# Kernel optimization log

Hardware: AMD Instinct MI355X
Metric: run time of the kernel (lower is better)

Reference implementation:

```python
import jax, jax.numpy as jnp
import numpy as np

EMBED_DIM = 512
NUM_HEADS = 8
HEAD_DIM = EMBED_DIM // NUM_HEADS
SCALE = 1.0 / HEAD_DIM ** 0.5


def setup_inputs() -> dict:
    key = jax.random.key(0)
    ks = jax.random.split(key, 7)
    B, C, H, W = 8, EMBED_DIM, 32, 32
    x = jax.random.normal(ks[0], (B, C, H, W), dtype=jnp.float32)
    s = 1.0 / np.sqrt(EMBED_DIM)
    return {
        "x": x,
        "ln_gamma": jnp.ones((EMBED_DIM,), jnp.float32),
        "ln_beta": jnp.zeros((EMBED_DIM,), jnp.float32),
        "w_qkv": jax.random.uniform(ks[1], (EMBED_DIM, 3 * EMBED_DIM), jnp.float32, -s, s),
        "b_qkv": jax.random.uniform(ks[2], (3 * EMBED_DIM,), jnp.float32, -s, s),
        "w_proj": jax.random.uniform(ks[3], (EMBED_DIM, EMBED_DIM), jnp.float32, -s, s),
        "b_proj": jax.random.uniform(ks[4], (EMBED_DIM,), jnp.float32, -s, s),
    }


def reference(x, ln_gamma, ln_beta, w_qkv, b_qkv, w_proj, b_proj):
    B, C, H, W = x.shape
    N = H * W
    # LayerNorm over channel dim (applied in NHWC layout in the original)
    xs = x.reshape(B, C, N).transpose(0, 2, 1)  # [B, N, C]
    mu = jnp.mean(xs, axis=-1, keepdims=True)
    var = jnp.mean(jnp.square(xs - mu), axis=-1, keepdims=True)
    xn = (xs - mu) / jnp.sqrt(var + 1e-5) * ln_gamma + ln_beta
    # QKV projection
    qkv = xn @ w_qkv + b_qkv                        # [B, N, 3C]
    qkv = qkv.reshape(B, N, 3, NUM_HEADS, HEAD_DIM)
    q = qkv[:, :, 0].transpose(0, 2, 1, 3)         # [B, h, N, d]
    k = qkv[:, :, 1].transpose(0, 2, 1, 3)
    v = qkv[:, :, 2].transpose(0, 2, 1, 3)
    # Scaled dot-product attention (full N x N scores, as in source)
    attn = jnp.einsum('bhnd,bhmd->bhnm', q, k) * SCALE
    attn = jax.nn.softmax(attn, axis=-1)
    o = jnp.einsum('bhnm,bhmd->bhnd', attn, v)     # [B, h, N, d]
    o = o.transpose(0, 2, 1, 3).reshape(B, N, C)
    # Output projection (dropout is identity in eval)
    o = o @ w_proj + b_proj
    return o.transpose(0, 2, 1).reshape(B, C, H, W)
```

## Files before the change

kernel.cpp:

```cpp
#include <hip/hip_runtime.h>
#include <hip/hip_bf16.h>
#include <math.h>

#define B_   8
#define C_   512
#define NH_  8
#define HD_  64
#define NSP  1024
#define M_   (B_*NSP)
#define NQKV 1536
#define SCALE_ 0.125f
#define S2L_  0.18033688f

typedef __attribute__((ext_vector_type(8))) __bf16 bf16x8;
typedef __attribute__((ext_vector_type(4))) float  f32x4;
typedef __attribute__((ext_vector_type(16))) float f32x16;

__device__ __forceinline__ unsigned short f2bf(float f) {
  unsigned int u = __float_as_uint(f);
  u = u + 0x7fffu + ((u >> 16) & 1u);
  return (unsigned short)(u >> 16);
}

__device__ __forceinline__ unsigned int pk2bf(float a, float b) {
  __hip_bfloat162 t = __float22bfloat162_rn(make_float2(a, b));
  unsigned int u; __builtin_memcpy(&u, &t, 4);
  return u;
}

__device__ __forceinline__ void async16(const unsigned short* g, unsigned short* l) {
  __builtin_amdgcn_global_load_lds(
      (const __attribute__((address_space(1))) void*)g,
      (__attribute__((address_space(3))) void*)l, 16, 0, 0);
}

__global__ void ln_stats_kernel(const float* __restrict__ x,
                                float* __restrict__ psum,
                                float* __restrict__ psum2) {
  int tx = threadIdx.x & 31, ty = threadIdx.x >> 5;
  int cg  = blockIdx.x & 3;
  int nch = (blockIdx.x >> 2) & 31;
  int b   = blockIdx.x >> 7;
  int n0 = nch * 32;
  const float* xp = x + (size_t)b * C_ * NSP + n0 + tx;
  float s = 0.f, s2 = 0.f;
  for (int c = cg * 128 + ty; c < cg * 128 + 128; c += 8) {
    float v = xp[(size_t)c * NSP];
    s += v; s2 += v * v;
  }
  __shared__ float sh_s[8][32], sh_s2[8][32];
  sh_s[ty][tx] = s; sh_s2[ty][tx] = s2;
  __syncthreads();
  if (ty == 0) {
    float S = 0.f, S2 = 0.f;
    for (int j = 0; j < 8; j++) { S += sh_s[j][tx]; S2 += sh_s2[j][tx]; }
    psum [cg * M_ + b * NSP + n0 + tx] = S;
    psum2[cg * M_ + b * NSP + n0 + tx] = S2;
  }
}

__global__ __launch_bounds__(256) void applyw_kernel(
    const float* __restrict__ x, const float* __restrict__ psum,
    const float* __restrict__ psum2, const float* __restrict__ gamma,
    const float* __restrict__ beta, const float* __restrict__ wqkv,
    const float* __restrict__ wproj, unsigned short* __restrict__ xn,
    unsigned short* __restrict__ wqkvT, unsigned short* __restrict__ wprojT) {
  int tid = threadIdx.x;
  __shared__ float tile[64][65];
  int tx = tid & 63, ty = tid >> 6;
  if (blockIdx.x >= 1024) {
    const float* W; unsigned short* WT; int NW, t;
    if (blockIdx.x < 1216) { W = wqkv;  WT = wqkvT;  NW = NQKV; t = blockIdx.x - 1024; }
    else                   { W = wproj; WT = wprojT; NW = C_;   t = blockIdx.x - 1216; }
    int ntiles = NW >> 6;
    int kt = t / ntiles, nt = t - kt * ntiles;
    for (int i = ty; i < 64; i += 4)
      tile[i][tx] = W[(size_t)(kt * 64 + i) * NW + nt * 64 + tx];
    __syncthreads();
    for (int i = ty; i < 64; i += 4)
      WT[(size_t)(nt * 64 + i) * C_ + kt * 64 + tx] = f2bf(tile[tx][i]);
    return;
  }
  __shared__ float smu[64], srs[64];
  int c0 = (blockIdx.x & 7) * 64;
  int n0 = ((blockIdx.x >> 3) & 15) * 64;
  int b  = blockIdx.x >> 7;
  if (tid < 64) {
    int n = b * NSP + n0 + tid;
    float s  = psum [n] + psum [M_ + n] + psum [2 * M_ + n] + psum [3 * M_ + n];
    float s2 = psum2[n] + psum2[M_ + n] + psum2[2 * M_ + n] + psum2[3 * M_ + n];
    float mu = s * (1.0f / C_);
    float var = s2 * (1.0f / C_) - mu * mu;
    smu[tid] = mu;
    srs[tid] = rsqrtf(var + 1e-5f);
  }
  const float* xp = x + ((size_t)b * C_ + c0) * NSP + n0;
  for (int i = ty; i < 64; i += 4)
    tile[i][tx] = xp[(size_t)i * NSP + tx];
  __syncthreads();
  float g = gamma[c0 + tx], be = beta[c0 + tx];
  unsigned short* op = xn + ((size_t)(b * NSP + n0)) * C_ + c0 + tx;
  for (int i = ty; i < 64; i += 4) {
    float v = (tile[tx][i] - smu[i]) * srs[i] * g + be;
    op[(size_t)i * C_] = f2bf(v);
  }
}

__global__ __launch_bounds__(256) void gemm_qkv_kernel(
    const unsigned short* __restrict__ A,
    const unsigned short* __restrict__ Bt,
    const float* __restrict__ bias,
    unsigned short* __restrict__ out0, unsigned short* __restrict__ out1) {
  __shared__ __align__(16) char smem[24576];
  int tid = threadIdx.x;
  int wave = tid >> 6, lane = tid & 63, quad = lane >> 4, l15 = lane & 15;
  int n0 = blockIdx.x * 128, m0 = blockIdx.y * 64;
  int wm = (wave >> 1) * 32, wn = (wave & 1) * 64;
  int srow = lane >> 2, schunk = (lane & 3) * 8;
  auto stage = [&](int k0, int buf) {
    unsigned short* As = (unsigned short*)(smem + buf * 12288);
    unsigned short* Bs = (unsigned short*)(smem + buf * 12288 + 4096);
    async16(A + (size_t)(m0 + wave * 16 + srow) * 512 + k0 + schunk,
            As + wave * 16 * 32 + lane * 8);
#pragma unroll
    for (int j = 0; j < 2; j++) {
      int r0 = (wave + 4 * j) * 16;
      async16(Bt + (size_t)(n0 + r0 + srow) * 512 + k0 + schunk, Bs + r0 * 32 + lane * 8);
    }
  };
  f32x4 acc[2][4] = {};
  stage(0, 0);
  for (int kt = 0; kt < 16; kt++) {
    int cur = kt & 1;
    __syncthreads();
    if (kt < 15) stage((kt + 1) * 32, cur ^ 1);
    unsigned short* As = (unsigned short*)(smem + cur * 12288);
    unsigned short* Bs = (unsigned short*)(smem + cur * 12288 + 4096);
    bf16x8 a[2], bb[4];
#pragma unroll
    for (int mt = 0; mt < 2; mt++)
      a[mt] = *(const bf16x8*)(As + (wm + mt * 16 + l15) * 32 + quad * 8);
#pragma unroll
    for (int nt = 0; nt < 4; nt++)
      bb[nt] = *(const bf16x8*)(Bs + (wn + nt * 16 + l15) * 32 + quad * 8);
#pragma unroll
    for (int mt = 0; mt < 2; mt++)
#pragma unroll
      for (int nt = 0; nt < 4; nt++)
        acc[mt][nt] = __builtin_amdgcn_mfma_f32_16x16x32_bf16(
            a[mt], bb[nt], acc[mt][nt], 0, 0, 0);
  }
  if (n0 < 1024) {
    float sc = ((n0 + wn) < 512) ? S2L_ : 1.0f;
#pragma unroll
    for (int mt = 0; mt < 2; mt++)
#pragma unroll
      for (int nt = 0; nt < 4; nt++)
#pragma unroll
        for (int r = 0; r < 4; r++) {
          int row = m0 + wm + mt * 16 + quad * 4 + r;
          int col = n0 + wn + nt * 16 + l15;
          out0[(size_t)row * 1024 + col] = f2bf((acc[mt][nt][r] + bias[col]) * sc);
        }
  } else {
    __syncthreads();
    unsigned short* buf = (unsigned short*)smem + wave * (32 * 17);
    int b = m0 >> 10, nbase = m0 & 1023;
    for (int nc = 0; nc < 4; nc++) {
#pragma unroll
      for (int mt = 0; mt < 2; mt++)
#pragma unroll
        for (int r = 0; r < 4; r++) {
          int col = n0 + wn + nc * 16 + l15;
          buf[(mt * 16 + quad * 4 + r) * 17 + l15] = f2bf(acc[mt][nc][r] + bias[col]);
        }
      int ml = lane & 31;
#pragma unroll
      for (int j = 0; j < 8; j++) {
        int cl = j * 2 + (lane >> 5);
        int crel = n0 - 1024 + wn + nc * 16 + cl;
        out1[((size_t)b * C_ + crel) * NSP + nbase + wm + ml] = buf[ml * 17 + cl];
      }
    }
  }
}

__global__ __launch_bounds__(256) void gemm_proj_kernel(
    const unsigned short* __restrict__ A,
    const unsigned short* __restrict__ Bt,
    const float* __restrict__ bias,
    float* __restrict__ O) {
  __shared__ __align__(16) char smem[20480];
  int tid = threadIdx.x;
  int wave = tid >> 6, lane = tid & 63, quad = lane >> 4, l15 = lane & 15;
  int n0 = blockIdx.x * 128, m0 = blockIdx.y * 32;
  int wm = (wave >> 1) * 16, wn = (wave & 1) * 64;
  int srow = lane >> 2, schunk = (lane & 3) * 8;
  auto stage = [&](int k0, int buf) {
    unsigned short* As = (unsigned short*)(smem + buf * 10240);
    unsigned short* Bs = (unsigned short*)(smem + buf * 10240 + 2048);
    if (wave < 2)
      async16(A + (size_t)(m0 + wave * 16 + srow) * 512 + k0 + schunk,
              As + wave * 16 * 32 + lane * 8);
#pragma unroll
    for (int j = 0; j < 2; j++) {
      int r0 = (wave + 4 * j) * 16;
      async16(Bt + (size_t)(n0 + r0 + srow) * 512 + k0 + schunk, Bs + r0 * 32 + lane * 8);
    }
  };
  f32x4 acc[4] = {};
  stage(0, 0);
  for (int kt = 0; kt < 16; kt++) {
    int cur = kt & 1;
    __syncthreads();
    if (kt < 15) stage((kt + 1) * 32, cur ^ 1);
    unsigned short* As = (unsigned short*)(smem + cur * 10240);
    unsigned short* Bs = (unsigned short*)(smem + cur * 10240 + 2048);
    bf16x8 a, bb[4];
    a = *(const bf16x8*)(As + (wm + l15) * 32 + quad * 8);
#pragma unroll
    for (int nt = 0; nt < 4; nt++)
      bb[nt] = *(const bf16x8*)(Bs + (wn + nt * 16 + l15) * 32 + quad * 8);
#pragma unroll
    for (int nt = 0; nt < 4; nt++)
      acc[nt] = __builtin_amdgcn_mfma_f32_16x16x32_bf16(a, bb[nt], acc[nt], 0, 0, 0);
  }
  __syncthreads();
  float* buf = (float*)smem + wave * (16 * 17);
  int b = m0 >> 10, nbase = m0 & 1023;
  int ml = lane & 15, cg = lane >> 4;
  for (int nc = 0; nc < 4; nc++) {
#pragma unroll
    for (int r = 0; r < 4; r++) {
      int col = n0 + wn + nc * 16 + l15;
      buf[(quad * 4 + r) * 17 + l15] = acc[nc][r] + bias[col];
    }
#pragma unroll
    for (int j = 0; j < 4; j++) {
      int cl = j * 4 + cg;
      int c = n0 + wn + nc * 16 + cl;
      O[((size_t)b * C_ + c) * NSP + nbase + wm + ml] = buf[ml * 17 + cl];
    }
  }
}

__global__ __launch_bounds__(256, 2) void attn_kernel(
    const unsigned short* __restrict__ qk,
    const unsigned short* __restrict__ vt,
    unsigned short* __restrict__ o_ws) {
  __shared__ __align__(16) unsigned short Ks[2][64][64];
  __shared__ __align__(16) unsigned short Vts[2][64][64];
  int tid = threadIdx.x;
  int wave = tid >> 6, lane = tid & 63;
  int l31 = lane & 31, hi = lane >> 5;
  int b = blockIdx.x >> 3, h = blockIdx.x & 7;
  int qb = blockIdx.y * 128 + wave * 32;
  int sc8 = lane & 7, sr8 = lane >> 3;
  int swz = sc8 ^ sr8;
  bf16x8 bq[4];
#pragma unroll
  for (int ks = 0; ks < 4; ks++)
    bq[ks] = *(const bf16x8*)(
        qk + (size_t)(b * NSP + qb + l31) * 1024 + h * 64 + ks * 16 + hi * 8);
  auto stage = [&](int it, int buf) {
    int k0 = it * 64;
#pragma unroll
    for (int g = 0; g < 2; g++) {
      int row = wave * 16 + g * 8 + sr8;
      async16(qk + (size_t)(b * NSP + k0 + row) * 1024 + 512 + h * 64 + swz * 8,
              &Ks[buf][wave * 16 + g * 8][0]);
      async16(vt + ((size_t)(b * C_ + h * 64 + row)) * NSP + k0 + swz * 8,
              &Vts[buf][wave * 16 + g * 8][0]);
    }
  };
  f32x16 ot0 = {}, ot1 = {};
  float lsum = 0.f;
  stage(0, 0);
  for (int it = 0; it < 16; it++) {
    int cur = it & 1;
    __syncthreads();
    if (it < 15) stage(it + 1, cur ^ 1);
    bf16x8 bp[4];
#pragma unroll
    for (int kt = 0; kt < 2; kt++) {
      f32x16 s = {};
#pragma unroll
      for (int ks = 0; ks < 4; ks++) {
        bf16x8 ak = *(const bf16x8*)(
            &Ks[cur][kt * 32 + l31][((ks * 2 + hi) ^ (l31 & 7)) * 8]);
        s = __builtin_amdgcn_mfma_f32_32x32x16_bf16(ak, bq[ks], s, 0, 0, 0);
      }
      float p0 = __builtin_amdgcn_exp2f(s[0]),  p1 = __builtin_amdgcn_exp2f(s[1]);
      float p2 = __builtin_amdgcn_exp2f(s[2]),  p3 = __builtin_amdgcn_exp2f(s[3]);
      float p4 = __builtin_amdgcn_exp2f(s[4]),  p5 = __builtin_amdgcn_exp2f(s[5]);
      float p6 = __builtin_amdgcn_exp2f(s[6]),  p7 = __builtin_amdgcn_exp2f(s[7]);
      float p8 = __builtin_amdgcn_exp2f(s[8]),  p9 = __builtin_amdgcn_exp2f(s[9]);
      float pa = __builtin_amdgcn_exp2f(s[10]), pb = __builtin_amdgcn_exp2f(s[11]);
      float pc = __builtin_amdgcn_exp2f(s[12]), pd = __builtin_amdgcn_exp2f(s[13]);
      float pe = __builtin_amdgcn_exp2f(s[14]), pf = __builtin_amdgcn_exp2f(s[15]);
      lsum += ((p0 + p1) + (p2 + p3)) + ((p4 + p5) + (p6 + p7)) +
              (((p8 + p9) + (pa + pb)) + ((pc + pd) + (pe + pf)));
      unsigned int d0 = pk2bf(p0, p1), d1 = pk2bf(p2, p3);
      unsigned int d2 = pk2bf(p4, p5), d3 = pk2bf(p6, p7);
      unsigned int d4 = pk2bf(p8, p9), d5 = pk2bf(pa, pb);
      unsigned int d6 = pk2bf(pc, pd), d7 = pk2bf(pe, pf);
      asm volatile("v_permlane32_swap_b32 %0, %1" : "+v"(d0), "+v"(d2));
      asm volatile("v_permlane32_swap_b32 %0, %1" : "+v"(d1), "+v"(d3));
      asm volatile("v_permlane32_swap_b32 %0, %1" : "+v"(d4), "+v"(d6));
      asm volatile("v_permlane32_swap_b32 %0, %1" : "+v"(d5), "+v"(d7));
      uint4 f0 = make_uint4(d0, d1, d2, d3);
      uint4 f1 = make_uint4(d4, d5, d6, d7);
      __builtin_memcpy(&bp[kt * 2 + 0], &f0, 16);
      __builtin_memcpy(&bp[kt * 2 + 1], &f1, 16);
    }
#pragma unroll
    for (int kc = 0; kc < 4; kc++) {
      bf16x8 av0 = *(const bf16x8*)(
          &Vts[cur][l31][((kc * 2 + hi) ^ (l31 & 7)) * 8]);
      ot0 = __builtin_amdgcn_mfma_f32_32x32x16_bf16(av0, bp[kc], ot0, 0, 0, 0);
      bf16x8 av1 = *(const bf16x8*)(
          &Vts[cur][32 + l31][(((kc * 2 + hi) ^ (l31 & 7)) ^ 0) * 8]);
      ot1 = __builtin_amdgcn_mfma_f32_32x32x16_bf16(av1, bp[kc], ot1, 0, 0, 0);
    }
  }
  float lv = __shfl(lsum, l31) + __shfl(lsum, l31 + 32);
  float inv = 1.f / lv;
  unsigned short* orow = o_ws + (size_t)(b * NSP + qb + l31) * 512 + h * 64;
#pragma unroll
  for (int g = 0; g < 4; g++) {
    int d0 = 8 * g + 4 * hi;
    *(uint2*)(orow + d0) =
        make_uint2(pk2bf(ot0[4 * g + 0] * inv, ot0[4 * g + 1] * inv),
                   pk2bf(ot0[4 * g + 2] * inv, ot0[4 * g + 3] * inv));
    *(uint2*)(orow + 32 + d0) =
        make_uint2(pk2bf(ot1[4 * g + 0] * inv, ot1[4 * g + 1] * inv),
                   pk2bf(ot1[4 * g + 2] * inv, ot1[4 * g + 3] * inv));
  }
}

extern "C" void kernel_launch(void* const* d_in, const int* in_sizes, int n_in,
                              void* d_out, int out_size, void* d_ws, size_t ws_size,
                              hipStream_t stream) {
  const float* x     = (const float*)d_in[0];
  const float* gamma = (const float*)d_in[1];
  const float* beta  = (const float*)d_in[2];
  const float* wqkv  = (const float*)d_in[3];
  const float* bqkv  = (const float*)d_in[4];
  const float* wproj = (const float*)d_in[5];
  const float* bproj = (const float*)d_in[6];
  char* ws = (char*)d_ws;
  float*          psum   = (float*)ws;
  float*          psum2  = (float*)(ws + 131072);
  unsigned short* wqkvT  = (unsigned short*)(ws + 262144);
  unsigned short* wprojT = (unsigned short*)(ws + 1835008);
  unsigned short* qk_bf  = (unsigned short*)(ws + 2359296);
  unsigned short* vt_bf  = (unsigned short*)(ws + 19136512);
  unsigned short* xn_bf  = (unsigned short*)(ws + 27525120);
  unsigned short* o_bf   = xn_bf;
  float* out = (float*)d_out;

  ln_stats_kernel<<<1024, 256, 0, stream>>>(x, psum, psum2);
  applyw_kernel<<<1024 + 192 + 64, 256, 0, stream>>>(x, psum, psum2, gamma, beta,
                                                     wqkv, wproj, xn_bf, wqkvT, wprojT);
  gemm_qkv_kernel<<<dim3(NQKV / 128, M_ / 64), 256, 0, stream>>>(
      xn_bf, wqkvT, bqkv, qk_bf, vt_bf);
  attn_kernel<<<dim3(B_ * NH_, NSP / 64 / 2), 256, 0, stream>>>(qk_bf, vt_bf, o_bf);
  gemm_proj_kernel<<<dim3(C_ / 128, M_ / 32), 256, 0, stream>>>(
      o_bf, wprojT, bproj, out);
}
```

Measured before the change: 155.6 us.

## Enlarge GEMM tiles and stage epilogue stores through shared memory

```diff
diff --git a/kernel.cpp b/kernel.cpp
--- a/kernel.cpp
+++ b/kernel.cpp
@@ -106,11 +106,101 @@
   }
 }
 
-__global__ __launch_bounds__(256) void gemm_qkv_kernel(
+__global__ __launch_bounds__(256, 3) void gemm_qkv_kernel(
     const unsigned short* __restrict__ A,
     const unsigned short* __restrict__ Bt,
     const float* __restrict__ bias,
     unsigned short* __restrict__ out0, unsigned short* __restrict__ out1) {
+  __shared__ __align__(16) char smem[32768];
+  int tid = threadIdx.x;
+  int wave = tid >> 6, lane = tid & 63, quad = lane >> 4, l15 = lane & 15;
+  int n0 = blockIdx.x * 128, m0 = blockIdx.y * 128;
+  int wm = (wave >> 1) * 64, wn = (wave & 1) * 64;
+  int srow = lane >> 2, schunk = (lane & 3) * 8;
+  auto stage = [&](int k0, int buf) {
+    unsigned short* As = (unsigned short*)(smem + buf * 16384);
+    unsigned short* Bs = (unsigned short*)(smem + buf * 16384 + 8192);
+#pragma unroll
+    for (int j = 0; j < 2; j++) {
+      int r0 = (wave + 4 * j) * 16;
+      async16(A + (size_t)(m0 + r0 + srow) * 512 + k0 + schunk, As + r0 * 32 + lane * 8);
+      async16(Bt + (size_t)(n0 + r0 + srow) * 512 + k0 + schunk, Bs + r0 * 32 + lane * 8);
+    }
+  };
+  f32x4 acc[4][4] = {};
+  stage(0, 0);
+  for (int kt = 0; kt < 16; kt++) {
+    int cur = kt & 1;
+    __syncthreads();
+    if (kt < 15) stage((kt + 1) * 32, cur ^ 1);
+    unsigned short* As = (unsigned short*)(smem + cur * 16384);
+    unsigned short* Bs = (unsigned short*)(smem + cur * 16384 + 8192);
+    bf16x8 a[4], bb[4];
+#pragma unroll
+    for (int mt = 0; mt < 4; mt++)
+      a[mt] = *(const bf16x8*)(As + (wm + mt * 16 + l15) * 32 + quad * 8);
+#pragma unroll
+    for (int nt = 0; nt < 4; nt++)
+      bb[nt] = *(const bf16x8*)(Bs + (wn + nt * 16 + l15) * 32 + quad * 8);
+#pragma unroll
+    for (int mt = 0; mt < 4; mt++)
+#pragma unroll
+      for (int nt = 0; nt < 4; nt++)
+        acc[mt][nt] = __builtin_amdgcn_mfma_f32_16x16x32_bf16(
+            a[mt], bb[nt], acc[mt][nt], 0, 0, 0);
+  }
+  __syncthreads();
+  float bw[4];
+#pragma unroll
+  for (int nt = 0; nt < 4; nt++) bw[nt] = bias[n0 + wn + nt * 16 + l15];
+  if (n0 < 1024) {
+    float sc = ((n0 + wn) < 512) ? S2L_ : 1.0f;
+    unsigned short* buf = (unsigned short*)(smem + wave * 8192);
+#pragma unroll
+    for (int p = 0; p < 2; p++) {
+#pragma unroll
+      for (int mh = 0; mh < 2; mh++) {
+        int mt = p * 2 + mh;
+#pragma unroll
+        for (int nt = 0; nt < 4; nt++)
+#pragma unroll
+          for (int r = 0; r < 4; r++)
+            buf[(mh * 16 + quad * 4 + r) * 68 + nt * 16 + l15] =
+                f2bf((acc[mt][nt][r] + bw[nt]) * sc);
+      }
+#pragma unroll
+      for (int i = 0; i < 4; i++) {
+        int row = i * 8 + (lane >> 3);
+        const unsigned short* bp_ = &buf[row * 68 + (lane & 7) * 8];
+        uint2 lo = *(const uint2*)bp_;
+        uint2 hi = *(const uint2*)(bp_ + 4);
+        *(uint4*)(out0 + (size_t)(m0 + wm + p * 32 + row) * 1024 +
+                  n0 + wn + (lane & 7) * 8) = make_uint4(lo.x, lo.y, hi.x, hi.y);
+      }
+    }
+  } else {
+    unsigned short* buf = (unsigned short*)(smem + wave * 8192);
+    int b = m0 >> 10, nbase = m0 & 1023;
+    for (int nc = 0; nc < 4; nc++) {
+#pragma unroll
+      for (int mt = 0; mt < 4; mt++)
+#pragma unroll
+        for (int r = 0; r < 4; r++)
+          buf[(mt * 16 + quad * 4 + r) * 17 + l15] = f2bf(acc[mt][nc][r] + bw[nc]);
+#pragma unroll
+      for (int cl = 0; cl < 16; cl++) {
+        int crel = n0 - 1024 + wn + nc * 16 + cl;
+        out1[((size_t)b * C_ + crel) * NSP + nbase + wm + lane] = buf[lane * 17 + cl];
+      }
+    }
+  }
+}
+
+__global__ __launch_bounds__(256) void gemm_proj_kernel(
+    const unsigned short* __restrict__ A,
+    const unsigned short* __restrict__ Bt,
+    const float* __restrict__ bias,
+    float* __restrict__ O) {
   __shared__ __align__(16) char smem[24576];
   int tid = threadIdx.x;
   int wave = tid >> 6, lane = tid & 63, quad = lane >> 4, l15 = lane & 15;
@@ -150,94 +240,22 @@
         acc[mt][nt] = __builtin_amdgcn_mfma_f32_16x16x32_bf16(
             a[mt], bb[nt], acc[mt][nt], 0, 0, 0);
   }
-  if (n0 < 1024) {
-    float sc = ((n0 + wn) < 512) ? S2L_ : 1.0f;
+  __syncthreads();
+  float bw[4];
+#pragma unroll
+  for (int nt = 0; nt < 4; nt++) bw[nt] = bias[n0 + wn + nt * 16 + l15];
+  float* buf = (float*)(smem + wave * 6144);
+  int b = m0 >> 10, nbase = m0 & 1023;
+  int ml = lane & 31, cg = lane >> 5;
+  for (int nc = 0; nc < 4; nc++) {
 #pragma unroll
     for (int mt = 0; mt < 2; mt++)
 #pragma unroll
-      for (int nt = 0; nt < 4; nt++)
-#pragma unroll
-        for (int r = 0; r < 4; r++) {
-          int row = m0 + wm + mt * 16 + quad * 4 + r;
-          int col = n0 + wn + nt * 16 + l15;
-          out0[(size_t)row * 1024 + col] = f2bf((acc[mt][nt][r] + bias[col]) * sc);
-        }
-  } else {
-    __syncthreads();
-    unsigned short* buf = (unsigned short*)smem + wave * (32 * 17);
-    int b = m0 >> 10, nbase = m0 & 1023;
-    for (int nc = 0; nc < 4; nc++) {
-#pragma unroll
-      for (int mt = 0; mt < 2; mt++)
-#pragma unroll
-        for (int r = 0; r < 4; r++) {
-          int col = n0 + wn + nc * 16 + l15;
-          buf[(mt * 16 + quad * 4 + r) * 17 + l15] = f2bf(acc[mt][nc][r] + bias[col]);
-        }
-      int ml = lane & 31;
-#pragma unroll
-      for (int j = 0; j < 8; j++) {
-        int cl = j * 2 + (lane >> 5);
-        int crel = n0 - 1024 + wn + nc * 16 + cl;
-        out1[((size_t)b * C_ + crel) * NSP + nbase + wm + ml] = buf[ml * 17 + cl];
-      }
-    }
-  }
-}
-
-__global__ __launch_bounds__(256) void gemm_proj_kernel(
-    const unsigned short* __restrict__ A,
-    const unsigned short* __restrict__ Bt,
-    const float* __restrict__ bias,
-    float* __restrict__ O) {
-  __shared__ __align__(16) char smem[20480];
-  int tid = threadIdx.x;
-  int wave = tid >> 6, lane = tid & 63, quad = lane >> 4, l15 = lane & 15;
-  int n0 = blockIdx.x * 128, m0 = blockIdx.y * 32;
-  int wm = (wave >> 1) * 16, wn = (wave & 1) * 64;
-  int srow = lane >> 2, schunk = (lane & 3) * 8;
-  auto stage = [&](int k0, int buf) {
-    unsigned short* As = (unsigned short*)(smem + buf * 10240);
-    unsigned short* Bs = (unsigned short*)(smem + buf * 10240 + 2048);
-    if (wave < 2)
-      async16(A + (size_t)(m0 + wave * 16 + srow) * 512 + k0 + schunk,
-              As + wave * 16 * 32 + lane * 8);
-#pragma unroll
-    for (int j = 0; j < 2; j++) {
-      int r0 = (wave + 4 * j) * 16;
-      async16(Bt + (size_t)(n0 + r0 + srow) * 512 + k0 + schunk, Bs + r0 * 32 + lane * 8);
-    }
-  };
-  f32x4 acc[4] = {};
-  stage(0, 0);
-  for (int kt = 0; kt < 16; kt++) {
-    int cur = kt & 1;
-    __syncthreads();
-    if (kt < 15) stage((kt + 1) * 32, cur ^ 1);
-    unsigned short* As = (unsigned short*)(smem + cur * 10240);
-    unsigned short* Bs = (unsigned short*)(smem + cur * 10240 + 2048);
-    bf16x8 a, bb[4];
-    a = *(const bf16x8*)(As + (wm + l15) * 32 + quad * 8);
-#pragma unroll
-    for (int nt = 0; nt < 4; nt++)
-      bb[nt] = *(const bf16x8*)(Bs + (wn + nt * 16 + l15) * 32 + quad * 8);
-#pragma unroll
-    for (int nt = 0; nt < 4; nt++)
-      acc[nt] = __builtin_amdgcn_mfma_f32_16x16x32_bf16(a, bb[nt], acc[nt], 0, 0, 0);
-  }
-  __syncthreads();
-  float* buf = (float*)smem + wave * (16 * 17);
-  int b = m0 >> 10, nbase = m0 & 1023;
-  int ml = lane & 15, cg = lane >> 4;
-  for (int nc = 0; nc < 4; nc++) {
-#pragma unroll
-    for (int r = 0; r < 4; r++) {
-      int col = n0 + wn + nc * 16 + l15;
-      buf[(quad * 4 + r) * 17 + l15] = acc[nc][r] + bias[col];
-    }
-#pragma unroll
-    for (int j = 0; j < 4; j++) {
-      int cl = j * 4 + cg;
+      for (int r = 0; r < 4; r++)
+        buf[(mt * 16 + quad * 4 + r) * 17 + l15] = acc[mt][nc][r] + bw[nc];
+#pragma unroll
+    for (int j = 0; j < 8; j++) {
+      int cl = j * 2 + cg;
       int c = n0 + wn + nc * 16 + cl;
       O[((size_t)b * C_ + c) * NSP + nbase + wm + ml] = buf[ml * 17 + cl];
     }
@@ -362,9 +380,9 @@
   ln_stats_kernel<<<1024, 256, 0, stream>>>(x, psum, psum2);
   applyw_kernel<<<1024 + 192 + 64, 256, 0, stream>>>(x, psum, psum2, gamma, beta,
                                                      wqkv, wproj, xn_bf, wqkvT, wprojT);
-  gemm_qkv_kernel<<<dim3(NQKV / 128, M_ / 64), 256, 0, stream>>>(
+  gemm_qkv_kernel<<<dim3(NQKV / 128, M_ / 128), 256, 0, stream>>>(
       xn_bf, wqkvT, bqkv, qk_bf, vt_bf);
   attn_kernel<<<dim3(B_ * NH_, NSP / 64 / 2), 256, 0, stream>>>(qk_bf, vt_bf, o_bf);
-  gemm_proj_kernel<<<dim3(C_ / 128, M_ / 32), 256, 0, stream>>>(
+  gemm_proj_kernel<<<dim3(C_ / 128, M_ / 64), 256, 0, stream>>>(
       o_bf, wprojT, bproj, out);
 }
```

After: 149.3 us. 4.0% less time.
